# Kernel optimization log

Hardware: AMD Instinct MI355X
Metric: run time of the kernel (lower is better)

Reference implementation:

```python
import jax, jax.numpy as jnp
import numpy as np
import math

H = 1024
E = 16
ENT_STRENGTH = 0.5
COHERENCE_TIME = 10.0
TIME_STEP = 0.0
K = 2
# static list of rotation pairs (i<j), applied sequentially as in the torch double loop
PAIRS = np.array([(i, j) for i in range(E) for j in range(i + 1, E)], dtype=np.int32)


def _mlp(x, w1, b1, w2, b2):
    h = jax.nn.gelu(x @ w1 + b1, approximate=False)  # torch default GELU = exact erf
    return h @ w2 + b2


def _apply_entanglement(amps, ent):
    # sequential Givens rotations over expert pairs; carry shape [B,S,E]
    pairs = jnp.asarray(PAIRS)

    def step(carry, pair):
        i, j = pair[0], pair[1]
        angle = ent[i, j] * ENT_STRENGTH
        c, s = jnp.cos(angle), jnp.sin(angle)
        ai = jnp.take(carry, i, axis=-1)  # [B,S]
        aj = jnp.take(carry, j, axis=-1)
        oh_i = jax.nn.one_hot(i, E, dtype=carry.dtype)
        oh_j = jax.nn.one_hot(j, E, dtype=carry.dtype)
        new = (carry * (1.0 - oh_i - oh_j)
               + (c * ai - s * aj)[..., None] * oh_i
               + (s * ai + c * aj)[..., None] * oh_j)
        return new, None

    out, _ = jax.lax.scan(step, amps, pairs)
    return out


def setup_inputs() -> dict:
    key = jax.random.key(0)
    ks = jax.random.split(key, 10)
    sc1 = 1.0 / math.sqrt(H)
    sc2 = 1.0 / math.sqrt(H // 2)
    return {
        "hidden_states": jax.random.normal(ks[0], (4, 4096, H), dtype=jnp.float32),
        "w1a": jax.random.uniform(ks[1], (H, H // 2), jnp.float32, -sc1, sc1),
        "b1a": jnp.zeros((H // 2,), jnp.float32),
        "w2a": jax.random.uniform(ks[2], (H // 2, E), jnp.float32, -sc2, sc2),
        "b2a": jnp.zeros((E,), jnp.float32),
        "w1p": jax.random.uniform(ks[3], (H, H // 2), jnp.float32, -sc1, sc1),
        "b1p": jnp.zeros((H // 2,), jnp.float32),
        "w2p": jax.random.uniform(ks[4], (H // 2, E), jnp.float32, -sc2, sc2),
        "b2p": jnp.zeros((E,), jnp.float32),
        "ent": jax.random.normal(ks[5], (E, E), dtype=jnp.float32) * 0.1,
    }


def reference(hidden_states, w1a, b1a, w2a, b2a, w1p, b1p, w2p, b2p, ent):
    raw_amps = _mlp(hidden_states, w1a, b1a, w2a, b2a)                 # [B,S,E]
    raw_phases = jnp.tanh(_mlp(hidden_states, w1p, b1p, w2p, b2p)) * jnp.float32(math.pi)
    amplitudes = jnp.sqrt(jax.nn.softmax(jnp.abs(raw_amps), axis=-1))
    entangled = _apply_entanglement(amplitudes, ent)
    coherence = jnp.exp(jnp.float32(-TIME_STEP / COHERENCE_TIME))      # time_step buffer = 0 -> 1.0
    decoherent = entangled * coherence
    probs = decoherent ** 2
    probs = probs / jnp.maximum(jnp.sum(jnp.abs(probs), axis=-1, keepdims=True), 1e-12)
    top_p, top_i = jax.lax.top_k(probs, K)
    top_p = top_p / jnp.maximum(jnp.sum(jnp.abs(top_p), axis=-1, keepdims=True), 1e-12)
    return top_p, top_i, decoherent, raw_phases, probs
```

## Files before the change

kernel.cpp:

```cpp
#include <hip/hip_runtime.h>
#include <math.h>

#define NTOK   16384
#define HDIM   1024
#define HHALF  512
#define NE     16

#define OFF_TP  0
#define OFF_TI  (NTOK * 2)
#define OFF_DEC (NTOK * 4)
#define OFF_PH  (OFF_DEC + NTOK * NE)
#define OFF_PR  (OFF_PH + NTOK * NE)

typedef _Float16 half8 __attribute__((ext_vector_type(8)));
typedef _Float16 half4 __attribute__((ext_vector_type(4)));
typedef float f32x16 __attribute__((ext_vector_type(16)));
typedef float f32x4 __attribute__((ext_vector_type(4)));

#define LO_SCALE     2048.0f
#define LO_SCALE_INV (1.0f / 2048.0f)
#define MFMA32(a,b,c) __builtin_amdgcn_mfma_f32_32x32x16_f16(a,b,c,0,0,0)
#define MFMA16(a,b,c) __builtin_amdgcn_mfma_f32_16x16x32_f16(a,b,c,0,0,0)

#define BAR() asm volatile("s_waitcnt lgkmcnt(0)\n\ts_barrier" ::: "memory")

__device__ __forceinline__ float gelu_exact(float x) {
    return 0.5f * x * (1.0f + erff(x * 0.70710678118654752440f));
}

__device__ __forceinline__ void cvt_split(float4 v, half4& hi, half4& lo) {
    _Float16 h0 = (_Float16)v.x, h1 = (_Float16)v.y,
             h2 = (_Float16)v.z, h3 = (_Float16)v.w;
    hi = (half4){h0, h1, h2, h3};
    lo = (half4){(_Float16)((v.x - (float)h0) * LO_SCALE),
                 (_Float16)((v.y - (float)h1) * LO_SCALE),
                 (_Float16)((v.z - (float)h2) * LO_SCALE),
                 (_Float16)((v.w - (float)h3) * LO_SCALE)};
}

__global__ void __launch_bounds__(256)
qir_wtrans(const float* __restrict__ w1a, const float* __restrict__ w1p,
           _Float16* __restrict__ wt, float* __restrict__ out)
{
    int u = blockIdx.x * 256 + threadIdx.x;
    out[OFF_PH + u] = 0.0f;
    out[OFF_PH + 262144 + u] = 0.0f;

    int l  = u & 63;
    int f  = (u >> 6) & 7;
    int sl = (u >> 9) & 7;
    int kc = (u >> 12) & 31;
    int ph = u >> 17;
    int nf = f >> 2, kh = (f >> 1) & 1, pl = f & 1;
    int col = sl * 64 + nf * 32 + (l & 31);
    int k0  = kc * 32 + kh * 16 + (l >> 5) * 8;
    const float* __restrict__ W = ph ? w1p : w1a;
    half8 v;
    #pragma unroll
    for (int j = 0; j < 8; ++j) {
        float x = W[(size_t)(k0 + j) * HHALF + col];
        _Float16 h = (_Float16)x;
        v[j] = pl ? (_Float16)((x - (float)h) * LO_SCALE) : h;
    }
    *(half8*)&wt[(size_t)u * 8] = v;
}

__global__ void __launch_bounds__(512, 2)
qir_gemm(const float* __restrict__ xg, const _Float16* __restrict__ wt,
         const float* __restrict__ b1a, const float* __restrict__ w2a, const float* __restrict__ b2a,
         const float* __restrict__ b1p, const float* __restrict__ w2p, const float* __restrict__ b2p,
         float* __restrict__ out)
{
    extern __shared__ char smem[];
    const int tid = threadIdx.x;
    const int l  = tid & 63;
    const int w  = tid >> 6;
    const int wm = w >> 2;
    const int wn = w & 3;
    const int bid  = blockIdx.x;
    const int mblk = bid & 127;
    const int v    = bid >> 7;
    const int ph   = v & 1;
    const int nh   = v >> 1;
    const int tok0 = mblk * 128;

    const float* __restrict__ b1 = ph ? b1p : b1a;
    const float* __restrict__ w2 = ph ? w2p : w2a;
    const float* __restrict__ b2 = ph ? b2p : b2a;
    const _Float16* __restrict__ wtp = wt + ((size_t)ph << 20);

    const int r  = tid >> 2;
    const int kq = tid & 3;
    const float* __restrict__ aptr = xg + (size_t)(tok0 + r) * HDIM + kq * 4;
    const int a_woff = (kq >> 1) * 2048 + r * 16 + (kq & 1) * 8;
    const int a_rd = (l >> 5) * 2048 + (wm * 64 + (l & 31)) * 16;

    const _Float16* __restrict__ bptr = wtp + (nh * 4 + wn) * 4096 + (size_t)l * 8;

    f32x16 a00{}, a01{}, a10{}, a11{}, c00{}, c01{}, c10{}, c11{};
    #pragma unroll
    for (int rg = 0; rg < 16; ++rg) {
        a00[rg] = 0.f; a01[rg] = 0.f; a10[rg] = 0.f; a11[rg] = 0.f;
        c00[rg] = 0.f; c01[rg] = 0.f; c10[rg] = 0.f; c11[rg] = 0.f;
    }

    half8 Bc[8], Bd[8];
    float4 xw[4];

    {
        #pragma unroll
        for (int c = 0; c < 4; ++c) {
            float4 vv = *(const float4*)(aptr + c * 16);
            half4 hv, lv;
            cvt_split(vv, hv, lv);
            *(half4*)(smem + a_woff + c * 4096) = hv;
            *(half4*)(smem + a_woff + c * 4096 + 16384) = lv;
        }
    }
    #pragma unroll
    for (int f = 0; f < 8; ++f) Bc[f] = *(const half8*)(bptr + f * 512);
    BAR();

    #pragma unroll 1
    for (int p = 0; p < 16; ++p) {
        char* const cur = smem + (p & 1) * 32768;
        char* const nxt = smem + ((p & 1) ^ 1) * 32768;

        #pragma unroll
        for (int f = 0; f < 8; ++f)
            Bd[f] = *(const half8*)(bptr + (size_t)(2 * p + 1) * 32768 + f * 512);
        if (p + 1 < 16) {
            #pragma unroll
            for (int c = 0; c < 4; ++c)
                xw[c] = *(const float4*)(aptr + (p + 1) * 64 + c * 16);
        }

        #pragma unroll
        for (int j = 0; j < 2; ++j) {
            const char* Aj = cur + j * 4096 + a_rd;
            half8 ah0 = *(const half8*)(Aj);
            half8 ah1 = *(const half8*)(Aj + 512);
            half8 al0 = *(const half8*)(Aj + 16384);
            half8 al1 = *(const half8*)(Aj + 16384 + 512);
            half8 bh0 = Bc[j * 2],     bl0 = Bc[j * 2 + 1];
            half8 bh1 = Bc[4 + j * 2], bl1 = Bc[4 + j * 2 + 1];
            a00 = MFMA32(ah0, bh0, a00); c00 = MFMA32(al0, bh0, c00); c00 = MFMA32(ah0, bl0, c00);
            a01 = MFMA32(ah0, bh1, a01); c01 = MFMA32(al0, bh1, c01); c01 = MFMA32(ah0, bl1, c01);
            a10 = MFMA32(ah1, bh0, a10); c10 = MFMA32(al1, bh0, c10); c10 = MFMA32(ah1, bl0, c10);
            a11 = MFMA32(ah1, bh1, a11); c11 = MFMA32(al1, bh1, c11); c11 = MFMA32(ah1, bl1, c11);
        }

        if (p + 1 < 16) {
            #pragma unroll
            for (int f = 0; f < 8; ++f)
                Bc[f] = *(const half8*)(bptr + (size_t)(2 * p + 2) * 32768 + f * 512);
        }

        #pragma unroll
        for (int j = 2; j < 4; ++j) {
            const char* Aj = cur + j * 4096 + a_rd;
            half8 ah0 = *(const half8*)(Aj);
            half8 ah1 = *(const half8*)(Aj + 512);
            half8 al0 = *(const half8*)(Aj + 16384);
            half8 al1 = *(const half8*)(Aj + 16384 + 512);
            const int kh = j - 2;
            half8 bh0 = Bd[kh * 2],     bl0 = Bd[kh * 2 + 1];
            half8 bh1 = Bd[4 + kh * 2], bl1 = Bd[4 + kh * 2 + 1];
            a00 = MFMA32(ah0, bh0, a00); c00 = MFMA32(al0, bh0, c00); c00 = MFMA32(ah0, bl0, c00);
            a01 = MFMA32(ah0, bh1, a01); c01 = MFMA32(al0, bh1, c01); c01 = MFMA32(ah0, bl1, c01);
            a10 = MFMA32(ah1, bh0, a10); c10 = MFMA32(al1, bh0, c10); c10 = MFMA32(ah1, bl0, c10);
            a11 = MFMA32(ah1, bh1, a11); c11 = MFMA32(al1, bh1, c11); c11 = MFMA32(ah1, bl1, c11);
        }

        if (p + 1 < 16) {
            #pragma unroll
            for (int c = 0; c < 4; ++c) {
                half4 hv, lv;
                cvt_split(xw[c], hv, lv);
                *(half4*)(nxt + a_woff + c * 4096) = hv;
                *(half4*)(nxt + a_woff + c * 4096 + 16384) = lv;
            }
        }
        BAR();
    }

    const int col0 = nh * 256 + wn * 64 + (l & 31);
    const float bb0 = b1[col0], bb1 = b1[col0 + 32];
    #pragma unroll
    for (int rg = 0; rg < 16; ++rg) {
        a00[rg] = gelu_exact(a00[rg] + c00[rg] * LO_SCALE_INV + bb0);
        a01[rg] = gelu_exact(a01[rg] + c01[rg] * LO_SCALE_INV + bb1);
        a10[rg] = gelu_exact(a10[rg] + c10[rg] * LO_SCALE_INV + bb0);
        a11[rg] = gelu_exact(a11[rg] + c11[rg] * LO_SCALE_INV + bb1);
    }

    char* const Hw = smem + w * 4096;
    char* const hb = Hw + ((l >> 3) & 3) * 1024 + (l & 7) * 2;
    float* const P = (float*)(smem + 32768);

    half8 w2h[2], w2l[2];
    #pragma unroll
    for (int nf = 0; nf < 2; ++nf) {
        #pragma unroll
        for (int j = 0; j < 8; ++j) {
            int kg = nh * 256 + wn * 64 + nf * 32 + (l >> 4) * 8 + j;
            float vv = w2[(size_t)kg * NE + (l & 15)];
            _Float16 hh = (_Float16)vv;
            w2h[nf][j] = hh;
            w2l[nf][j] = (_Float16)((vv - (float)hh) * LO_SCALE);
        }
    }

    f32x4 acc2[4], acc2s[4];
    #pragma unroll
    for (int m16 = 0; m16 < 4; ++m16)
        #pragma unroll
        for (int rg = 0; rg < 4; ++rg) { acc2[m16][rg] = 0.f; acc2s[m16][rg] = 0.f; }

#define H2PASS(ACC0, ACC1, NF, PL)                                             \
    {                                                                          \
        _Pragma("unroll")                                                      \
        for (int rg = 0; rg < 16; ++rg) {                                      \
            int row0 = (rg & 3) + 8 * (rg >> 2) + 4 * (l >> 5);                \
            { float vv = ACC0[rg]; _Float16 hh = (_Float16)vv;                 \
              *(_Float16*)(hb + row0 * 16) =                                   \
                  (PL) ? (_Float16)(vv - (float)hh) : hh; }                    \
            { float vv = ACC1[rg]; _Float16 hh = (_Float16)vv;                 \
              *(_Float16*)(hb + (32 + row0) * 16) =                            \
                  (PL) ? (_Float16)(vv - (float)hh) : hh; }                    \
        }                                                                      \
        _Pragma("unroll")                                                      \
        for (int m16 = 0; m16 < 4; ++m16) {                                    \
            half8 a2 = *(const half8*)(Hw + (l >> 4) * 1024 +                  \
                                       (m16 * 16 + (l & 15)) * 16);            \
            acc2[m16] = MFMA16(a2, w2h[NF], acc2[m16]);                        \
            if (!(PL)) acc2s[m16] = MFMA16(a2, w2l[NF], acc2s[m16]);           \
        }                                                                      \
    }

    H2PASS(a00, a10, 0, 0)
    H2PASS(a01, a11, 1, 0)
    H2PASS(a00, a10, 0, 1)
    H2PASS(a01, a11, 1, 1)
#undef H2PASS

    #pragma unroll
    for (int m16 = 0; m16 < 4; ++m16)
        #pragma unroll
        for (int rg = 0; rg < 4; ++rg) {
            int row = m16 * 16 + ((l >> 4) << 2) + rg;
            P[w * 1024 + row * 16 + (l & 15)] =
                acc2[m16][rg] + acc2s[m16][rg] * LO_SCALE_INV;
        }
    __syncthreads();

    #pragma unroll
    for (int rep = 0; rep < 4; ++rep) {
        int oi = tid + rep * 512;
        int t = oi >> 4, e = oi & 15;
        int bw = (t >> 6) * 4, tl = t & 63;
        float sum = 0.5f * b2[e]
                  + P[(bw + 0) * 1024 + tl * 16 + e]
                  + P[(bw + 1) * 1024 + tl * 16 + e]
                  + P[(bw + 2) * 1024 + tl * 16 + e]
                  + P[(bw + 3) * 1024 + tl * 16 + e];
        atomicAdd(out + (ph ? OFF_PH : OFF_PR) + (size_t)(tok0 + t) * NE + e, sum);
    }
}

__global__ void __launch_bounds__(512)
qir_mlp(const float* __restrict__ xg,
        const float* __restrict__ w1a, const float* __restrict__ b1a,
        const float* __restrict__ w2a, const float* __restrict__ b2a,
        const float* __restrict__ w1p, const float* __restrict__ b1p,
        const float* __restrict__ w2p, const float* __restrict__ b2p,
        float* __restrict__ out)
{
    __shared__ float sh_w[16][HHALF];
    __shared__ float sh_x[16][68];

    const int tid  = threadIdx.x;
    const int cg   = tid & 63;
    const int tg   = tid >> 6;
    const int tok0 = blockIdx.x * 64;
    const int cA   = cg * 4;
    const int cB   = 256 + cg * 4;

    for (int phase = 0; phase < 2; ++phase) {
        const float* __restrict__ w1 = phase ? w1p : w1a;
        const float* __restrict__ b1 = phase ? b1p : b1a;
        const float* __restrict__ w2 = phase ? w2p : w2a;
        const float* __restrict__ b2 = phase ? b2p : b2a;

        float acc[8][8];
        #pragma unroll
        for (int t = 0; t < 8; ++t)
            #pragma unroll
            for (int c = 0; c < 8; ++c) acc[t][c] = 0.0f;

        float4 wreg[4];
        float4 xreg = make_float4(0.f, 0.f, 0.f, 0.f);

        auto load_chunk = [&](int kc) {
            #pragma unroll
            for (int p = 0; p < 4; ++p) {
                int f  = tid + p * 512;
                int k  = f >> 7;
                int c4 = (f & 127) << 2;
                wreg[p] = *(const float4*)&w1[(kc * 16 + k) * HHALF + c4];
            }
            if (tid < 256) {
                int t  = tid >> 2;
                int k4 = (tid & 3) << 2;
                xreg = *(const float4*)&xg[(size_t)(tok0 + t) * HDIM + kc * 16 + k4];
            }
        };

        load_chunk(0);
        for (int kc = 0; kc < HDIM / 16; ++kc) {
            __syncthreads();
            #pragma unroll
            for (int p = 0; p < 4; ++p) {
                int f  = tid + p * 512;
                int k  = f >> 7;
                int c4 = (f & 127) << 2;
                *(float4*)&sh_w[k][c4] = wreg[p];
            }
            if (tid < 256) {
                int t  = tid >> 2;
                int k4 = (tid & 3) << 2;
                sh_x[k4 + 0][t] = xreg.x;
                sh_x[k4 + 1][t] = xreg.y;
                sh_x[k4 + 2][t] = xreg.z;
                sh_x[k4 + 3][t] = xreg.w;
            }
            __syncthreads();
            if (kc + 1 < HDIM / 16) load_chunk(kc + 1);

            #pragma unroll 4
            for (int k = 0; k < 16; ++k) {
                float4 xa = *(const float4*)&sh_x[k][tg * 8];
                float4 xb = *(const float4*)&sh_x[k][tg * 8 + 4];
                float4 wa = *(const float4*)&sh_w[k][cA];
                float4 wb = *(const float4*)&sh_w[k][cB];
                float xs[8] = {xa.x, xa.y, xa.z, xa.w, xb.x, xb.y, xb.z, xb.w};
                float ws[8] = {wa.x, wa.y, wa.z, wa.w, wb.x, wb.y, wb.z, wb.w};
                #pragma unroll
                for (int t = 0; t < 8; ++t)
                    #pragma unroll
                    for (int c = 0; c < 8; ++c)
                        acc[t][c] = fmaf(xs[t], ws[c], acc[t][c]);
            }
        }

        {
            float4 bA4 = *(const float4*)&b1[cA];
            float4 bB4 = *(const float4*)&b1[cB];
            float bs[8] = {bA4.x, bA4.y, bA4.z, bA4.w, bB4.x, bB4.y, bB4.z, bB4.w};
            #pragma unroll
            for (int t = 0; t < 8; ++t)
                #pragma unroll
                for (int c = 0; c < 8; ++c)
                    acc[t][c] = gelu_exact(acc[t][c] + bs[c]);
        }

        for (int e = 0; e < NE; ++e) {
            float w2v[8];
            #pragma unroll
            for (int j = 0; j < 4; ++j) {
                w2v[j]     = w2[(cA + j) * NE + e];
                w2v[4 + j] = w2[(cB + j) * NE + e];
            }
            float bias2 = b2[e];
            #pragma unroll
            for (int t = 0; t < 8; ++t) {
                float s = 0.0f;
                #pragma unroll
                for (int j = 0; j < 8; ++j) s = fmaf(acc[t][j], w2v[j], s);
                #pragma unroll
                for (int off = 1; off < 64; off <<= 1)
                    s += __shfl_xor(s, off, 64);
                if (cg == 0) {
                    float raw   = s + bias2;
                    int   token = tok0 + tg * 8 + t;
                    out[(phase ? OFF_PH : OFF_PR) + (size_t)token * NE + e] = raw;
                }
            }
        }
    }
}

__global__ void __launch_bounds__(256)
qir_epilogue(const float* __restrict__ ent, float* __restrict__ out)
{
    __shared__ float sh_c[120], sh_s[120];
    const int tid = threadIdx.x;
    if (tid < 120) {
        int rem = tid, i = 0;
        while (rem >= 15 - i) { rem -= 15 - i; ++i; }
        int j = i + 1 + rem;
        float ang = ent[i * NE + j] * 0.5f;
        sh_c[tid] = cosf(ang);
        sh_s[tid] = sinf(ang);
    }
    __syncthreads();

    const int token = blockIdx.x * 256 + tid;

    #pragma unroll
    for (int q = 0; q < 4; ++q) {
        float4 v = *(const float4*)&out[OFF_PH + (size_t)token * NE + q * 4];
        v.x = tanhf(v.x) * 3.14159265358979323846f;
        v.y = tanhf(v.y) * 3.14159265358979323846f;
        v.z = tanhf(v.z) * 3.14159265358979323846f;
        v.w = tanhf(v.w) * 3.14159265358979323846f;
        *(float4*)&out[OFF_PH + (size_t)token * NE + q * 4] = v;
    }

    float a[16];
    #pragma unroll
    for (int q = 0; q < 4; ++q) {
        float4 v = *(const float4*)&out[OFF_PR + (size_t)token * NE + q * 4];
        a[q*4+0] = v.x; a[q*4+1] = v.y; a[q*4+2] = v.z; a[q*4+3] = v.w;
    }

    float m = fabsf(a[0]);
    #pragma unroll
    for (int e = 1; e < 16; ++e) m = fmaxf(m, fabsf(a[e]));
    float ssum = 0.0f;
    #pragma unroll
    for (int e = 0; e < 16; ++e) { a[e] = expf(fabsf(a[e]) - m); ssum += a[e]; }
    float inv = 1.0f / ssum;
    #pragma unroll
    for (int e = 0; e < 16; ++e) a[e] = sqrtf(a[e] * inv);

    {
        int p = 0;
        #pragma unroll
        for (int i = 0; i < 16; ++i) {
            #pragma unroll
            for (int j = i + 1; j < 16; ++j) {
                float c = sh_c[p], s = sh_s[p]; ++p;
                float ai = a[i], aj = a[j];
                a[i] = c * ai - s * aj;
                a[j] = s * ai + c * aj;
            }
        }
    }

    #pragma unroll
    for (int q = 0; q < 4; ++q)
        *(float4*)&out[OFF_DEC + (size_t)token * NE + q * 4] =
            make_float4(a[q*4], a[q*4+1], a[q*4+2], a[q*4+3]);

    float pr[16];
    float s2 = 0.0f;
    #pragma unroll
    for (int e = 0; e < 16; ++e) { pr[e] = a[e] * a[e]; s2 += pr[e]; }
    float inv2 = 1.0f / fmaxf(s2, 1e-12f);
    #pragma unroll
    for (int e = 0; e < 16; ++e) pr[e] *= inv2;
    #pragma unroll
    for (int q = 0; q < 4; ++q)
        *(float4*)&out[OFF_PR + (size_t)token * NE + q * 4] =
            make_float4(pr[q*4], pr[q*4+1], pr[q*4+2], pr[q*4+3]);

    float bv = pr[0]; int bi = 0;
    #pragma unroll
    for (int e = 1; e < 16; ++e) if (pr[e] > bv) { bv = pr[e]; bi = e; }
    float sv = -1.0f; int si = 0;
    #pragma unroll
    for (int e = 0; e < 16; ++e) if (e != bi && pr[e] > sv) { sv = pr[e]; si = e; }
    float ts = fmaxf(fabsf(bv) + fabsf(sv), 1e-12f);
    out[OFF_TP + (size_t)token * 2 + 0] = bv / ts;
    out[OFF_TP + (size_t)token * 2 + 1] = sv / ts;
    out[OFF_TI + (size_t)token * 2 + 0] = (float)bi;
    out[OFF_TI + (size_t)token * 2 + 1] = (float)si;
}

extern "C" void kernel_launch(void* const* d_in, const int* in_sizes, int n_in,
                              void* d_out, int out_size, void* d_ws, size_t ws_size,
                              hipStream_t stream) {
    const float* xg  = (const float*)d_in[0];
    const float* w1a = (const float*)d_in[1];
    const float* b1a = (const float*)d_in[2];
    const float* w2a = (const float*)d_in[3];
    const float* b2a = (const float*)d_in[4];
    const float* w1p = (const float*)d_in[5];
    const float* b1p = (const float*)d_in[6];
    const float* w2p = (const float*)d_in[7];
    const float* b2p = (const float*)d_in[8];
    const float* ent = (const float*)d_in[9];
    float* out = (float*)d_out;

    if (ws_size >= (size_t)4 * 1024 * 1024) {
        _Float16* wt = (_Float16*)d_ws;
        qir_wtrans<<<1024, 256, 0, stream>>>(w1a, w1p, wt, out);
        qir_gemm<<<512, 512, 65536, stream>>>(xg, wt, b1a, w2a, b2a,
                                              b1p, w2p, b2p, out);
    } else {
        qir_mlp<<<NTOK / 64, 512, 0, stream>>>(xg, w1a, b1a, w2a, b2a,
                                               w1p, b1p, w2p, b2p, out);
    }
    qir_epilogue<<<NTOK / 256, 256, 0, stream>>>(ent, out);
}
```

Measured before the change: 136.5 us.

## Restructure split-precision GEMM: full-N tiles, bf16 residual terms, async LDS B loads

```diff
diff --git a/kernel.cpp b/kernel.cpp
--- a/kernel.cpp
+++ b/kernel.cpp
@@ -14,24 +14,52 @@
 
 typedef _Float16 half8 __attribute__((ext_vector_type(8)));
 typedef _Float16 half4 __attribute__((ext_vector_type(4)));
+typedef short    bf16x8 __attribute__((ext_vector_type(8)));
 typedef float f32x16 __attribute__((ext_vector_type(16)));
 typedef float f32x4 __attribute__((ext_vector_type(4)));
 
+typedef __attribute__((address_space(3))) void lds_void_t;
+typedef const __attribute__((address_space(1))) void gbl_void_t;
+
 #define LO_SCALE     2048.0f
 #define LO_SCALE_INV (1.0f / 2048.0f)
-#define MFMA32(a,b,c) __builtin_amdgcn_mfma_f32_32x32x16_f16(a,b,c,0,0,0)
-#define MFMA16(a,b,c) __builtin_amdgcn_mfma_f32_16x16x32_f16(a,b,c,0,0,0)
+#define MFMA_F16(a,b,c)  __builtin_amdgcn_mfma_f32_32x32x16_f16(a,b,c,0,0,0)
+#define MFMA_BF16(a,b,c) __builtin_amdgcn_mfma_f32_32x32x16_bf16(a,b,c,0,0,0)
+#define MFMA16(a,b,c)    __builtin_amdgcn_mfma_f32_16x16x32_f16(a,b,c,0,0,0)
 
 #define BAR() asm volatile("s_waitcnt lgkmcnt(0)\n\ts_barrier" ::: "memory")
+#define SB()  __builtin_amdgcn_sched_barrier(0)
+
+#define WSB_PER_PH  (64 * 16384)
+#define WSL_BASE    2097152
+#define WSL_PER_PH  (64 * 8192)
+#define WS_BYTES    ((size_t)(2097152 + 1048576) * 2)
 
 __device__ __forceinline__ float gelu_exact(float x) {
     return 0.5f * x * (1.0f + erff(x * 0.70710678118654752440f));
 }
 
-__device__ __forceinline__ void cvt_split(float4 v, half4& hi, half4& lo) {
+__device__ __forceinline__ short f32_to_bf16_bits(float f) {
+    unsigned u = __builtin_bit_cast(unsigned, f);
+    u += 0x7FFFu + ((u >> 16) & 1u);
+    return (short)(u >> 16);
+}
+__device__ __forceinline__ float bf16_bits_to_f32(short s) {
+    unsigned u = ((unsigned)(unsigned short)s) << 16;
+    return __builtin_bit_cast(float, u);
+}
+__device__ __forceinline__ bf16x8 cvt_h2b(half8 h) {
+    bf16x8 r;
+    #pragma unroll
+    for (int j = 0; j < 8; ++j) r[j] = f32_to_bf16_bits((float)h[j]);
+    return r;
+}
+__device__ __forceinline__ void cvt_splitQ(float4 v, half4& hi, half4& lo) {
     _Float16 h0 = (_Float16)v.x, h1 = (_Float16)v.y,
              h2 = (_Float16)v.z, h3 = (_Float16)v.w;
-    hi = (half4){h0, h1, h2, h3};
+    const _Float16 S = (_Float16)2048.0f;
+    hi = (half4){(_Float16)(h0 * S), (_Float16)(h1 * S),
+                 (_Float16)(h2 * S), (_Float16)(h3 * S)};
     lo = (half4){(_Float16)((v.x - (float)h0) * LO_SCALE),
                  (_Float16)((v.y - (float)h1) * LO_SCALE),
                  (_Float16)((v.z - (float)h2) * LO_SCALE),
@@ -40,29 +68,51 @@
 
 __global__ void __launch_bounds__(256)
 qir_wtrans(const float* __restrict__ w1a, const float* __restrict__ w1p,
-           _Float16* __restrict__ wt, float* __restrict__ out)
+           _Float16* __restrict__ wt)
 {
     int u = blockIdx.x * 256 + threadIdx.x;
-    out[OFF_PH + u] = 0.0f;
-    out[OFF_PH + 262144 + u] = 0.0f;
-
-    int l  = u & 63;
-    int f  = (u >> 6) & 7;
-    int sl = (u >> 9) & 7;
-    int kc = (u >> 12) & 31;
-    int ph = u >> 17;
-    int nf = f >> 2, kh = (f >> 1) & 1, pl = f & 1;
-    int col = sl * 64 + nf * 32 + (l & 31);
-    int k0  = kc * 32 + kh * 16 + (l >> 5) * 8;
-    const float* __restrict__ W = ph ? w1p : w1a;
-    half8 v;
-    #pragma unroll
-    for (int j = 0; j < 8; ++j) {
-        float x = W[(size_t)(k0 + j) * HHALF + col];
-        _Float16 h = (_Float16)x;
-        v[j] = pl ? (_Float16)((x - (float)h) * LO_SCALE) : h;
-    }
-    *(half8*)&wt[(size_t)u * 8] = v;
+    short* wt16 = (short*)wt;
+    if (u < 262144) {
+        int l   = u & 63;
+        int pl  = (u >> 6) & 1;
+        int c32 = (u >> 7) & 15;
+        int hk  = (u >> 11) & 63;
+        int ph  = u >> 17;
+        int col = c32 * 32 + (l & 31);
+        int k0  = hk * 16 + (l >> 5) * 8;
+        const float* __restrict__ W = ph ? w1p : w1a;
+        short v[8];
+        #pragma unroll
+        for (int j = 0; j < 8; ++j) {
+            float x = W[(size_t)(k0 + j) * HHALF + col];
+            _Float16 h = (_Float16)x;
+            if (pl == 0) v[j] = __builtin_bit_cast(short, h);
+            else         v[j] = f32_to_bf16_bits(x - (float)h);
+        }
+        #pragma unroll
+        for (int j = 0; j < 8; ++j) wt16[(size_t)u * 8 + j] = v[j];
+    } else {
+        int u2  = u - 262144;
+        int l   = u2 & 63;
+        int c32 = (u2 >> 6) & 15;
+        int hk  = (u2 >> 10) & 63;
+        int ph  = u2 >> 16;
+        int col = c32 * 32 + (l & 31);
+        int k0  = hk * 16 + (l >> 5) * 8;
+        const float* __restrict__ W = ph ? w1p : w1a;
+        short v[8];
+        #pragma unroll
+        for (int j = 0; j < 8; ++j) {
+            float x = W[(size_t)(k0 + j) * HHALF + col];
+            _Float16 h = (_Float16)x;
+            float r1 = x - (float)h;
+            short lob = f32_to_bf16_bits(r1);
+            float r2 = r1 - bf16_bits_to_f32(lob);
+            v[j] = f32_to_bf16_bits(r2);
+        }
+        #pragma unroll
+        for (int j = 0; j < 8; ++j) wt16[(size_t)WSL_BASE + (size_t)u2 * 8 + j] = v[j];
+    }
 }
 
 __global__ void __launch_bounds__(512, 2)
@@ -79,137 +129,128 @@
     const int wn = w & 3;
     const int bid  = blockIdx.x;
     const int mblk = bid & 127;
-    const int v    = bid >> 7;
-    const int ph   = v & 1;
-    const int nh   = v >> 1;
+    const int ph   = bid >> 7;
     const int tok0 = mblk * 128;
 
     const float* __restrict__ b1 = ph ? b1p : b1a;
     const float* __restrict__ w2 = ph ? w2p : w2a;
     const float* __restrict__ b2 = ph ? b2p : b2a;
-    const _Float16* __restrict__ wtp = wt + ((size_t)ph << 20);
+    const _Float16* __restrict__ wsB = wt + (size_t)ph * WSB_PER_PH;
+    const _Float16* __restrict__ wsL = wt + WSL_BASE + (size_t)ph * WSL_PER_PH;
+
+    char* const Bb0 = smem + 32768;
+    char* const Bb1 = smem + 65536;
 
     const int r  = tid >> 2;
     const int kq = tid & 3;
     const float* __restrict__ aptr = xg + (size_t)(tok0 + r) * HDIM + kq * 4;
-    const int a_woff = (kq >> 1) * 2048 + r * 16 + (kq & 1) * 8;
-    const int a_rd = (l >> 5) * 2048 + (wm * 64 + (l & 31)) * 16;
-
-    const _Float16* __restrict__ bptr = wtp + (nh * 4 + wn) * 4096 + (size_t)l * 8;
-
-    f32x16 a00{}, a01{}, a10{}, a11{}, c00{}, c01{}, c10{}, c11{};
-    #pragma unroll
-    for (int rg = 0; rg < 16; ++rg) {
-        a00[rg] = 0.f; a01[rg] = 0.f; a10[rg] = 0.f; a11[rg] = 0.f;
-        c00[rg] = 0.f; c01[rg] = 0.f; c10[rg] = 0.f; c11[rg] = 0.f;
-    }
-
-    half8 Bc[8], Bd[8];
-    float4 xw[4];
+    const int a_w  = (kq >> 1) * 4096 + r * 16 + (kq & 1) * 8;
+    const int a_rd = (l >> 5) * 4096 + (wm * 64 + (l & 31)) * 16;
+
+    f32x16 acc[2][4];
+    #pragma unroll
+    for (int m = 0; m < 2; ++m)
+        #pragma unroll
+        for (int nf = 0; nf < 4; ++nf)
+            #pragma unroll
+            for (int rg = 0; rg < 16; ++rg) acc[m][nf][rg] = 0.0f;
+
+    bf16x8 lloA[4], lloB[4];
+    float4 xw0, xw1;
+
+    auto stageA = [&](char* An, float4 v0, float4 v1) {
+        half4 hv, lv;
+        cvt_splitQ(v0, hv, lv);
+        *(half4*)(An + a_w) = hv;
+        *(half4*)(An + a_w + 2048) = lv;
+        cvt_splitQ(v1, hv, lv);
+        *(half4*)(An + 8192 + a_w) = hv;
+        *(half4*)(An + 8192 + a_w + 2048) = lv;
+    };
+    auto gldsB = [&](int hkn, char* Bn) {
+        const _Float16* src = wsB + (size_t)hkn * 16384 + (w * 4) * 512 + l * 8;
+        char* dst = Bn + (w * 4) * 1024;
+        #pragma unroll
+        for (int q = 0; q < 4; ++q)
+            __builtin_amdgcn_global_load_lds((gbl_void_t*)(src + q * 512),
+                                             (lds_void_t*)(dst + q * 1024), 16, 0, 0);
+    };
+    auto loadLLO = [&](int hkn, bf16x8 (&d)[4]) {
+        #pragma unroll
+        for (int nf = 0; nf < 4; ++nf)
+            d[nf] = *(const bf16x8*)(wsL + ((size_t)hkn * 16 + (wn * 4 + nf)) * 512 + l * 8);
+    };
 
     {
-        #pragma unroll
-        for (int c = 0; c < 4; ++c) {
-            float4 vv = *(const float4*)(aptr + c * 16);
-            half4 hv, lv;
-            cvt_split(vv, hv, lv);
-            *(half4*)(smem + a_woff + c * 4096) = hv;
-            *(half4*)(smem + a_woff + c * 4096 + 16384) = lv;
-        }
-    }
-    #pragma unroll
-    for (int f = 0; f < 8; ++f) Bc[f] = *(const half8*)(bptr + f * 512);
-    BAR();
+        float4 v0 = *(const float4*)(aptr);
+        float4 v1 = *(const float4*)(aptr + 16);
+        stageA(smem, v0, v1);
+        gldsB(0, Bb0);
+        loadLLO(0, lloA);
+        __syncthreads();
+    }
+
+    auto halfStep = [&](int hk, int kh, char* Ac, char* An, char* Bc, char* Bn,
+                        bf16x8 (&lc)[4], bf16x8 (&ln)[4], int p) {
+        const bool even = (kh == 0);
+        if (hk + 1 < 64) { gldsB(hk + 1, Bn); }
+        SB();
+        if (hk + 1 < 64) { loadLLO(hk + 1, ln); }
+        SB();
+        if (even && p + 1 < 32) {
+            xw0 = *(const float4*)(aptr + (p + 1) * 32);
+            xw1 = *(const float4*)(aptr + (p + 1) * 32 + 16);
+        }
+        SB();
+        const char* Abase = Ac + a_rd + kh * 8192;
+        half8 xh0 = *(const half8*)(Abase);
+        half8 xl0 = *(const half8*)(Abase + 2048);
+        half8 xh1 = *(const half8*)(Abase + 512);
+        half8 xl1 = *(const half8*)(Abase + 512 + 2048);
+        bf16x8 xb0 = cvt_h2b(xh0);
+        bf16x8 xb1 = cvt_h2b(xh1);
+        #pragma unroll
+        for (int nf = 0; nf < 4; ++nf) {
+            const char* Bbase = Bc + ((wn * 4 + nf) * 2) * 1024 + l * 16;
+            half8  wh  = *(const half8*)(Bbase);
+            bf16x8 wlo = *(const bf16x8*)(Bbase + 1024);
+            acc[0][nf] = MFMA_F16(xh0, wh, acc[0][nf]);
+            acc[1][nf] = MFMA_F16(xh1, wh, acc[1][nf]);
+            acc[0][nf] = MFMA_F16(xl0, wh, acc[0][nf]);
+            acc[1][nf] = MFMA_F16(xl1, wh, acc[1][nf]);
+            acc[0][nf] = MFMA_BF16(xb0, wlo, acc[0][nf]);
+            acc[1][nf] = MFMA_BF16(xb1, wlo, acc[1][nf]);
+            acc[0][nf] = MFMA_BF16(xb0, lc[nf], acc[0][nf]);
+            acc[1][nf] = MFMA_BF16(xb1, lc[nf], acc[1][nf]);
+        }
+        if (!even && p + 1 < 32) stageA(An, xw0, xw1);
+        if (even) asm volatile("s_waitcnt vmcnt(6)" ::: "memory");
+        else      asm volatile("s_waitcnt vmcnt(4)" ::: "memory");
+        BAR();
+    };
 
     #pragma unroll 1
-    for (int p = 0; p < 16; ++p) {
-        char* const cur = smem + (p & 1) * 32768;
-        char* const nxt = smem + ((p & 1) ^ 1) * 32768;
-
-        #pragma unroll
-        for (int f = 0; f < 8; ++f)
-            Bd[f] = *(const half8*)(bptr + (size_t)(2 * p + 1) * 32768 + f * 512);
-        if (p + 1 < 16) {
-            #pragma unroll
-            for (int c = 0; c < 4; ++c)
-                xw[c] = *(const float4*)(aptr + (p + 1) * 64 + c * 16);
-        }
-
-        #pragma unroll
-        for (int j = 0; j < 2; ++j) {
-            const char* Aj = cur + j * 4096 + a_rd;
-            half8 ah0 = *(const half8*)(Aj);
-            half8 ah1 = *(const half8*)(Aj + 512);
-            half8 al0 = *(const half8*)(Aj + 16384);
-            half8 al1 = *(const half8*)(Aj + 16384 + 512);
-            half8 bh0 = Bc[j * 2],     bl0 = Bc[j * 2 + 1];
-            half8 bh1 = Bc[4 + j * 2], bl1 = Bc[4 + j * 2 + 1];
-            a00 = MFMA32(ah0, bh0, a00); c00 = MFMA32(al0, bh0, c00); c00 = MFMA32(ah0, bl0, c00);
-            a01 = MFMA32(ah0, bh1, a01); c01 = MFMA32(al0, bh1, c01); c01 = MFMA32(ah0, bl1, c01);
-            a10 = MFMA32(ah1, bh0, a10); c10 = MFMA32(al1, bh0, c10); c10 = MFMA32(ah1, bl0, c10);
-            a11 = MFMA32(ah1, bh1, a11); c11 = MFMA32(al1, bh1, c11); c11 = MFMA32(ah1, bl1, c11);
-        }
-
-        if (p + 1 < 16) {
-            #pragma unroll
-            for (int f = 0; f < 8; ++f)
-                Bc[f] = *(const half8*)(bptr + (size_t)(2 * p + 2) * 32768 + f * 512);
-        }
-
-        #pragma unroll
-        for (int j = 2; j < 4; ++j) {
-            const char* Aj = cur + j * 4096 + a_rd;
-            half8 ah0 = *(const half8*)(Aj);
-            half8 ah1 = *(const half8*)(Aj + 512);
-            half8 al0 = *(const half8*)(Aj + 16384);
-            half8 al1 = *(const half8*)(Aj + 16384 + 512);
-            const int kh = j - 2;
-            half8 bh0 = Bd[kh * 2],     bl0 = Bd[kh * 2 + 1];
-            half8 bh1 = Bd[4 + kh * 2], bl1 = Bd[4 + kh * 2 + 1];
-            a00 = MFMA32(ah0, bh0, a00); c00 = MFMA32(al0, bh0, c00); c00 = MFMA32(ah0, bl0, c00);
-            a01 = MFMA32(ah0, bh1, a01); c01 = MFMA32(al0, bh1, c01); c01 = MFMA32(ah0, bl1, c01);
-            a10 = MFMA32(ah1, bh0, a10); c10 = MFMA32(al1, bh0, c10); c10 = MFMA32(ah1, bl0, c10);
-            a11 = MFMA32(ah1, bh1, a11); c11 = MFMA32(al1, bh1, c11); c11 = MFMA32(ah1, bl1, c11);
-        }
-
-        if (p + 1 < 16) {
-            #pragma unroll
-            for (int c = 0; c < 4; ++c) {
-                half4 hv, lv;
-                cvt_split(xw[c], hv, lv);
-                *(half4*)(nxt + a_woff + c * 4096) = hv;
-                *(half4*)(nxt + a_woff + c * 4096 + 16384) = lv;
-            }
-        }
-        BAR();
-    }
-
-    const int col0 = nh * 256 + wn * 64 + (l & 31);
-    const float bb0 = b1[col0], bb1 = b1[col0 + 32];
-    #pragma unroll
-    for (int rg = 0; rg < 16; ++rg) {
-        a00[rg] = gelu_exact(a00[rg] + c00[rg] * LO_SCALE_INV + bb0);
-        a01[rg] = gelu_exact(a01[rg] + c01[rg] * LO_SCALE_INV + bb1);
-        a10[rg] = gelu_exact(a10[rg] + c10[rg] * LO_SCALE_INV + bb0);
-        a11[rg] = gelu_exact(a11[rg] + c11[rg] * LO_SCALE_INV + bb1);
-    }
+    for (int p = 0; p < 32; ++p) {
+        char* Ac = smem + (p & 1) * 16384;
+        char* An = smem + ((p + 1) & 1) * 16384;
+        halfStep(2 * p,     0, Ac, An, Bb0, Bb1, lloA, lloB, p);
+        halfStep(2 * p + 1, 1, Ac, An, Bb1, Bb0, lloB, lloA, p);
+    }
+
+    float bcol[4];
+    #pragma unroll
+    for (int nf = 0; nf < 4; ++nf) bcol[nf] = b1[wn * 128 + nf * 32 + (l & 31)];
+    #pragma unroll
+    for (int m = 0; m < 2; ++m)
+        #pragma unroll
+        for (int nf = 0; nf < 4; ++nf)
+            #pragma unroll
+            for (int rg = 0; rg < 16; ++rg)
+                acc[m][nf][rg] = gelu_exact(acc[m][nf][rg] * LO_SCALE_INV + bcol[nf]);
 
     char* const Hw = smem + w * 4096;
     char* const hb = Hw + ((l >> 3) & 3) * 1024 + (l & 7) * 2;
     float* const P = (float*)(smem + 32768);
-
-    half8 w2h[2], w2l[2];
-    #pragma unroll
-    for (int nf = 0; nf < 2; ++nf) {
-        #pragma unroll
-        for (int j = 0; j < 8; ++j) {
-            int kg = nh * 256 + wn * 64 + nf * 32 + (l >> 4) * 8 + j;
-            float vv = w2[(size_t)kg * NE + (l & 15)];
-            _Float16 hh = (_Float16)vv;
-            w2h[nf][j] = hh;
-            w2l[nf][j] = (_Float16)((vv - (float)hh) * LO_SCALE);
-        }
-    }
 
     f32x4 acc2[4], acc2s[4];
     #pragma unroll
@@ -238,10 +279,25 @@
         }                                                                      \
     }
 
-    H2PASS(a00, a10, 0, 0)
-    H2PASS(a01, a11, 1, 0)
-    H2PASS(a00, a10, 0, 1)
-    H2PASS(a01, a11, 1, 1)
+    #pragma unroll
+    for (int ch = 0; ch < 2; ++ch) {
+        half8 w2h[2], w2l[2];
+        #pragma unroll
+        for (int nf2 = 0; nf2 < 2; ++nf2) {
+            #pragma unroll
+            for (int j = 0; j < 8; ++j) {
+                int kg = wn * 128 + ch * 64 + nf2 * 32 + (l >> 4) * 8 + j;
+                float vv = w2[(size_t)kg * NE + (l & 15)];
+                _Float16 hh = (_Float16)vv;
+                w2h[nf2][j] = hh;
+                w2l[nf2][j] = (_Float16)((vv - (float)hh) * LO_SCALE);
+            }
+        }
+        H2PASS(acc[0][ch * 2 + 0], acc[1][ch * 2 + 0], 0, 0)
+        H2PASS(acc[0][ch * 2 + 1], acc[1][ch * 2 + 1], 1, 0)
+        H2PASS(acc[0][ch * 2 + 0], acc[1][ch * 2 + 0], 0, 1)
+        H2PASS(acc[0][ch * 2 + 1], acc[1][ch * 2 + 1], 1, 1)
+    }
 #undef H2PASS
 
     #pragma unroll
@@ -258,13 +314,13 @@
     for (int rep = 0; rep < 4; ++rep) {
         int oi = tid + rep * 512;
         int t = oi >> 4, e = oi & 15;
-        int bw = (t >> 6) * 4, tl = t & 63;
-        float sum = 0.5f * b2[e]
-                  + P[(bw + 0) * 1024 + tl * 16 + e]
-                  + P[(bw + 1) * 1024 + tl * 16 + e]
-                  + P[(bw + 2) * 1024 + tl * 16 + e]
-                  + P[(bw + 3) * 1024 + tl * 16 + e];
-        atomicAdd(out + (ph ? OFF_PH : OFF_PR) + (size_t)(tok0 + t) * NE + e, sum);
+        int mh = t >> 6, tl = t & 63;
+        float sum = b2[e]
+                  + P[(mh * 4 + 0) * 1024 + tl * 16 + e]
+                  + P[(mh * 4 + 1) * 1024 + tl * 16 + e]
+                  + P[(mh * 4 + 2) * 1024 + tl * 16 + e]
+                  + P[(mh * 4 + 3) * 1024 + tl * 16 + e];
+        out[(ph ? OFF_PH : OFF_PR) + (size_t)(tok0 + t) * NE + e] = sum;
     }
 }
 
@@ -493,10 +549,10 @@
     const float* ent = (const float*)d_in[9];
     float* out = (float*)d_out;
 
-    if (ws_size >= (size_t)4 * 1024 * 1024) {
+    if (ws_size >= WS_BYTES) {
         _Float16* wt = (_Float16*)d_ws;
-        qir_wtrans<<<1024, 256, 0, stream>>>(w1a, w1p, wt, out);
-        qir_gemm<<<512, 512, 65536, stream>>>(xg, wt, b1a, w2a, b2a,
+        qir_wtrans<<<1536, 256, 0, stream>>>(w1a, w1p, wt);
+        qir_gemm<<<256, 512, 98304, stream>>>(xg, wt, b1a, w2a, b2a,
                                               b1p, w2p, b2p, out);
     } else {
         qir_mlp<<<NTOK / 64, 512, 0, stream>>>(xg, w1a, b1a, w2a, b2a,
```

Result: slower. 256.1 us (+87.7%).
